# Performance work log

Hardware: AMD Instinct MI355X
Metric: run time of the kernel (lower is better)

The kernel has to match this reference:

```python
import jax, jax.numpy as jnp
import numpy as np
import math

PI = math.pi
TWO_PI = 2.0 * math.pi
RESCALE = 2.0 * math.pi  # stand-in for dataset.rescale(FdFoRefAngle): normalized -> radians


def clamp_angle(angle):
    # |angle| mod 2pi, folded into [0, pi]
    a = jnp.abs(angle) % TWO_PI
    return jnp.where(a > PI, TWO_PI - a, a)


def setup_inputs() -> dict:
    key = jax.random.key(0)
    k1, k2 = jax.random.split(key)
    B = 8388608
    prediction = jax.random.normal(k1, (B, 3), dtype=jnp.float32)
    label = jax.random.normal(k2, (B, 3), dtype=jnp.float32)
    return {"prediction": prediction, "label": label}


def reference(prediction, label):
    pred_angle = prediction[:, 2] * RESCALE
    label_angle = label[:, 2] * RESCALE
    angle_diff = clamp_angle(pred_angle - label_angle) / PI  # [B]
    angle_diff = angle_diff[:, None]                          # [B, 1]
    pred_vector = jnp.concatenate([prediction[:, :2], angle_diff], axis=1)   # [B, 3]
    label_vector = jnp.concatenate([label[:, :2], jnp.zeros_like(angle_diff)], axis=1)
    # MSELoss(reduction='sum')
    return jnp.sum((pred_vector - label_vector) ** 2)
```

## Files before the change

kernel.cpp:

```cpp
#include <hip/hip_runtime.h>

constexpr int BLOCKS = 768;
constexpr int TPB    = 256;

__global__ __launch_bounds__(TPB) void loss_partial_kernel(
    const float* __restrict__ pred,
    const float* __restrict__ lab,
    float* __restrict__ partial,
    long long n4,
    long long n_elems)
{
    const long long tid = (long long)blockIdx.x * blockDim.x + threadIdx.x;
    const long long S   = (long long)gridDim.x * blockDim.x;

    const float4* __restrict__ p4 = (const float4*)pred;
    const float4* __restrict__ l4 = (const float4*)lab;

    const int m = (int)(tid % 3);
    bool isang[4];
#pragma unroll
    for (int k = 0; k < 4; ++k) isang[k] = (((m + k) % 3) == 2);

    float acc = 0.0f;

    const long long iters = n4 / (S * 4);
    long long q = tid;
    for (long long it = 0; it < iters; ++it) {
        float4 pv[4], lv[4];
#pragma unroll
        for (int u = 0; u < 4; ++u) {
            pv[u] = p4[q + (long long)u * S];
            lv[u] = l4[q + (long long)u * S];
        }
#pragma unroll
        for (int u = 0; u < 4; ++u) {
            const float* pp = (const float*)&pv[u];
            const float* ll = (const float*)&lv[u];
#pragma unroll
            for (int k = 0; k < 4; ++k) {
                float d = pp[k] - ll[k];
                float x = fabsf(d);
                float f = x - floorf(x);
                float t = 2.0f * fminf(f, 1.0f - f);
                float v = isang[k] ? t : d;
                acc = fmaf(v, v, acc);
            }
        }
        q += 4 * S;
    }

    for (; q < n4; q += S) {
        float4 pvr = p4[q];
        float4 lvr = l4[q];
        const float* pp = (const float*)&pvr;
        const float* ll = (const float*)&lvr;
#pragma unroll
        for (int k = 0; k < 4; ++k) {
            float d = pp[k] - ll[k];
            float x = fabsf(d);
            float f = x - floorf(x);
            float t = 2.0f * fminf(f, 1.0f - f);
            float v = isang[k] ? t : d;
            acc = fmaf(v, v, acc);
        }
    }

    const long long tail_base = n4 * 4;
    if (tid < n_elems - tail_base) {
        long long e = tail_base + tid;
        float d = pred[e] - lab[e];
        if ((int)(e % 3) == 2) {
            float x = fabsf(d);
            float f = x - floorf(x);
            d = 2.0f * fminf(f, 1.0f - f);
        }
        acc = fmaf(d, d, acc);
    }

#pragma unroll
    for (int off = 32; off > 0; off >>= 1)
        acc += __shfl_down(acc, off, 64);

    __shared__ float s_partial[TPB / 64];
    const int lane = threadIdx.x & 63;
    const int wave = threadIdx.x >> 6;
    if (lane == 0) s_partial[wave] = acc;
    __syncthreads();

    if (threadIdx.x == 0) {
        float v = 0.0f;
#pragma unroll
        for (int w = 0; w < TPB / 64; ++w) v += s_partial[w];
        partial[blockIdx.x] = v;
    }
}

__global__ __launch_bounds__(TPB) void reduce_partials_kernel(
    const float* __restrict__ partial, float* __restrict__ out, int n)
{
    float acc = 0.0f;
    for (int i = threadIdx.x; i < n; i += TPB) acc += partial[i];

#pragma unroll
    for (int off = 32; off > 0; off >>= 1)
        acc += __shfl_down(acc, off, 64);

    __shared__ float s_partial[TPB / 64];
    const int lane = threadIdx.x & 63;
    const int wave = threadIdx.x >> 6;
    if (lane == 0) s_partial[wave] = acc;
    __syncthreads();

    if (threadIdx.x == 0) {
        float v = 0.0f;
#pragma unroll
        for (int w = 0; w < TPB / 64; ++w) v += s_partial[w];
        out[0] = v;
    }
}

extern "C" void kernel_launch(void* const* d_in, const int* in_sizes, int n_in,
                              void* d_out, int out_size, void* d_ws, size_t ws_size,
                              hipStream_t stream) {
    const float* pred = (const float*)d_in[0];
    const float* lab  = (const float*)d_in[1];
    float* out = (float*)d_out;
    float* partial = (float*)d_ws;

    long long n_elems = (long long)in_sizes[0];
    long long n4 = n_elems / 4;

    loss_partial_kernel<<<BLOCKS, TPB, 0, stream>>>(pred, lab, partial, n4, n_elems);
    reduce_partials_kernel<<<1, TPB, 0, stream>>>(partial, out, BLOCKS);
}
```

Before: 212.1 us.

## Replace persistent grid-stride loop with one block per 512 rows and vectorized final reduce

The main kernel no longer uses a fixed grid of 768 blocks with a 4x-unrolled grid-stride loop. It now launches enough blocks that each thread handles two float4 chunks, raising occupancy and memory-level parallelism for this streaming reduction. The final reduce grows to 1024 threads and reads the partials as float4, since there are now far more of them. In exchange the partial buffer in the workspace becomes much larger, which may exceed ws_size. The angle mask is also recomputed from a 64-bit modulo for each chunk.

Result: no change. 213.3 us (+0.6%).

```diff
diff --git a/kernel.cpp b/kernel.cpp
--- a/kernel.cpp
+++ b/kernel.cpp
@@ -1,7 +1,24 @@
 #include <hip/hip_runtime.h>
 
-constexpr int BLOCKS = 768;
-constexpr int TPB    = 256;
+constexpr int TPB  = 256;
+constexpr int TPB2 = 1024;
+
+__device__ __forceinline__ float row_contrib(float4 pv, float4 lv, int m) {
+    const float* pp = (const float*)&pv;
+    const float* ll = (const float*)&lv;
+    float acc = 0.0f;
+#pragma unroll
+    for (int k = 0; k < 4; ++k) {
+        float d = pp[k] - ll[k];
+        float x = fabsf(d);
+        float f = x - floorf(x);
+        float t = 2.0f * fminf(f, 1.0f - f);
+        bool ang = (((m + k) % 3) == 2);
+        float v = ang ? t : d;
+        acc = fmaf(v, v, acc);
+    }
+    return acc;
+}
 
 __global__ __launch_bounds__(TPB) void loss_partial_kernel(
     const float* __restrict__ pred,
@@ -16,53 +33,27 @@
     const float4* __restrict__ p4 = (const float4*)pred;
     const float4* __restrict__ l4 = (const float4*)lab;
 
-    const int m = (int)(tid % 3);
-    bool isang[4];
-#pragma unroll
-    for (int k = 0; k < 4; ++k) isang[k] = (((m + k) % 3) == 2);
-
     float acc = 0.0f;
 
-    const long long iters = n4 / (S * 4);
-    long long q = tid;
-    for (long long it = 0; it < iters; ++it) {
-        float4 pv[4], lv[4];
-#pragma unroll
-        for (int u = 0; u < 4; ++u) {
-            pv[u] = p4[q + (long long)u * S];
-            lv[u] = l4[q + (long long)u * S];
+    const long long q0 = tid;
+    const long long q1 = tid + S;
+
+    if (q1 < n4) {
+        float4 pa = p4[q0];
+        float4 la = l4[q0];
+        float4 pb = p4[q1];
+        float4 lb = l4[q1];
+        acc += row_contrib(pa, la, (int)(q0 % 3));
+        acc += row_contrib(pb, lb, (int)(q1 % 3));
+        for (long long q = tid + 2 * S; q < n4; q += S) {
+            float4 pv = p4[q];
+            float4 lv = l4[q];
+            acc += row_contrib(pv, lv, (int)(q % 3));
         }
-#pragma unroll
-        for (int u = 0; u < 4; ++u) {
-            const float* pp = (const float*)&pv[u];
-            const float* ll = (const float*)&lv[u];
-#pragma unroll
-            for (int k = 0; k < 4; ++k) {
-                float d = pp[k] - ll[k];
-                float x = fabsf(d);
-                float f = x - floorf(x);
-                float t = 2.0f * fminf(f, 1.0f - f);
-                float v = isang[k] ? t : d;
-                acc = fmaf(v, v, acc);
-            }
-        }
-        q += 4 * S;
-    }
-
-    for (; q < n4; q += S) {
-        float4 pvr = p4[q];
-        float4 lvr = l4[q];
-        const float* pp = (const float*)&pvr;
-        const float* ll = (const float*)&lvr;
-#pragma unroll
-        for (int k = 0; k < 4; ++k) {
-            float d = pp[k] - ll[k];
-            float x = fabsf(d);
-            float f = x - floorf(x);
-            float t = 2.0f * fminf(f, 1.0f - f);
-            float v = isang[k] ? t : d;
-            acc = fmaf(v, v, acc);
-        }
+    } else if (q0 < n4) {
+        float4 pv = p4[q0];
+        float4 lv = l4[q0];
+        acc += row_contrib(pv, lv, (int)(q0 % 3));
     }
 
     const long long tail_base = n4 * 4;
@@ -95,17 +86,24 @@
     }
 }
 
-__global__ __launch_bounds__(TPB) void reduce_partials_kernel(
+__global__ __launch_bounds__(TPB2) void reduce_partials_kernel(
     const float* __restrict__ partial, float* __restrict__ out, int n)
 {
     float acc = 0.0f;
-    for (int i = threadIdx.x; i < n; i += TPB) acc += partial[i];
+    const int n4p = n / 4;
+    const float4* __restrict__ p4 = (const float4*)partial;
+    for (int i = threadIdx.x; i < n4p; i += TPB2) {
+        float4 v = p4[i];
+        acc += (v.x + v.y) + (v.z + v.w);
+    }
+    for (int i = n4p * 4 + threadIdx.x; i < n; i += TPB2)
+        acc += partial[i];
 
 #pragma unroll
     for (int off = 32; off > 0; off >>= 1)
         acc += __shfl_down(acc, off, 64);
 
-    __shared__ float s_partial[TPB / 64];
+    __shared__ float s_partial[TPB2 / 64];
     const int lane = threadIdx.x & 63;
     const int wave = threadIdx.x >> 6;
     if (lane == 0) s_partial[wave] = acc;
@@ -114,7 +112,7 @@
     if (threadIdx.x == 0) {
         float v = 0.0f;
 #pragma unroll
-        for (int w = 0; w < TPB / 64; ++w) v += s_partial[w];
+        for (int w = 0; w < TPB2 / 64; ++w) v += s_partial[w];
         out[0] = v;
     }
 }
@@ -130,6 +128,9 @@
     long long n_elems = (long long)in_sizes[0];
     long long n4 = n_elems / 4;
 
-    loss_partial_kernel<<<BLOCKS, TPB, 0, stream>>>(pred, lab, partial, n4, n_elems);
-    reduce_partials_kernel<<<1, TPB, 0, stream>>>(partial, out, BLOCKS);
+    int blocks = (int)((n4 + 2LL * TPB - 1) / (2LL * TPB));
+    if (blocks < 1) blocks = 1;
+
+    loss_partial_kernel<<<blocks, TPB, 0, stream>>>(pred, lab, partial, n4, n_elems);
+    reduce_partials_kernel<<<1, TPB2, 0, stream>>>(partial, out, blocks);
 }
```
